# Optimization experiments

Hardware: AMD Instinct MI355X
Metric: run time of the kernel (lower is better)

## Reference

```python
import jax, jax.numpy as jnp
import numpy as np

B, L, VOCAB = 2, 1024, 32000
D = 512            # latent_dim
NL = 2             # num_layers
INNER = 2 * D      # mamba_expand * latent_dim
MLP = 2048         # mlp_inner_dim
NSEG = 8           # fixed number of subsequences (segment starts every SEG tokens)
SEG = L // NSEG


def setup_inputs() -> dict:
    key = jax.random.key(0)
    ks = jax.random.split(key, 12)
    decoder_output = jax.random.normal(ks[0], (B, L, VOCAB), jnp.float32) * 0.02
    input_ids = jax.random.randint(ks[1], (B, L, 1), 0, VOCAB)
    segmentation_indices = jnp.zeros((B, L, 1), jnp.int32).at[:, jnp.arange(0, L, SEG), :].set(1)
    E = jax.random.normal(ks[2], (VOCAB, D), jnp.float32) * 0.02          # tied embedding
    A = jax.random.uniform(ks[3], (NL, INNER), jnp.float32, 0.9, 0.999)   # per-channel SSM decay
    Win = jax.random.normal(ks[4], (NL, D, 2 * INNER), jnp.float32) * (D ** -0.5)
    Wout = jax.random.normal(ks[5], (NL, INNER, D), jnp.float32) * (INNER ** -0.5)
    Wm1 = jax.random.normal(ks[6], (NL, D, MLP), jnp.float32) * (D ** -0.5)
    Wm2 = jax.random.normal(ks[7], (NL, MLP, D), jnp.float32) * (MLP ** -0.5)
    mu_W = jax.random.normal(ks[8], (D, D), jnp.float32) * (D ** -0.5)
    mu_b = jnp.zeros((D,), jnp.float32)
    lv_W = jax.random.normal(ks[9], (D, D), jnp.float32) * (D ** -0.5)
    lv_b = jnp.zeros((D,), jnp.float32)
    return dict(decoder_output=decoder_output, input_ids=input_ids,
                segmentation_indices=segmentation_indices, E=E, A=A, Win=Win,
                Wout=Wout, Wm1=Wm1, Wm2=Wm2, mu_W=mu_W, mu_b=mu_b, lv_W=lv_W, lv_b=lv_b)


def _recurrence(a, u):
    # linear SSM recurrence h_t = a * h_{t-1} + u_t ; u: (..., L, INNER)
    u_t = jnp.moveaxis(u, -2, 0)
    h0 = jnp.zeros(u_t.shape[1:], u.dtype)
    def step(h, ut):
        h = a * h + ut
        return h, h
    _, hs = jax.lax.scan(step, h0, u_t)
    return jnp.moveaxis(hs, 0, -2)


def _seq_mixer(x, A, Win, Wout, Wm1, Wm2):
    # causal Mamba-style encoder: gated linear recurrence block + MLP block, residual
    for l in range(NL):
        u, g = jnp.split(x @ Win[l], 2, axis=-1)
        h = _recurrence(A[l], u)
        x = x + (jax.nn.silu(g) * h) @ Wout[l]
        x = x + jax.nn.silu(x @ Wm1[l]) @ Wm2[l]
    return x


def reference(decoder_output, input_ids, segmentation_indices, E, A, Win, Wout, Wm1, Wm2, mu_W, mu_b, lv_W, lv_b):
    correct = E[input_ids[..., 0]]                          # (B,L,D) ground-truth embeddings
    dec = jnp.einsum('blv,vd->bld', decoder_output, E)      # tied-linear projection of logits
    mask = segmentation_indices[..., 0].astype(bool)        # (B,L)
    starts = jax.vmap(lambda m: jnp.nonzero(m, size=NSEG)[0])(mask)        # (B,NSEG)
    ends = jnp.concatenate([starts[:, 1:], jnp.full((B, 1), L, starts.dtype)], axis=1)
    pos = jnp.arange(L)
    use_c = pos[None, None, :] < starts[:, :, None]                        # context region
    use_d = (pos[None, None, :] >= starts[:, :, None]) & (pos[None, None, :] < ends[:, :, None])
    # subsequence i = correct-embedding context [0,start_i) ++ decoder segment [start_i,end_i), zero-padded to L
    x = jnp.where(use_c[..., None], correct[:, None], 0.0) + jnp.where(use_d[..., None], dec[:, None], 0.0)  # (B,NSEG,L,D)
    h = _seq_mixer(x, A, Win, Wout, Wm1, Wm2)
    idx = (ends - 1)[:, :, None, None]                                     # last valid position per subsequence
    last = jnp.take_along_axis(h, idx, axis=2)[:, :, 0, :]                 # (B,NSEG,D)
    mu_q = last @ mu_W + mu_b
    logvar_q = last @ lv_W + lv_b
    return mu_q, logvar_q
```

## Files before the change

### kernel.cpp

```cpp
#include <hip/hip_runtime.h>
#include <hip/hip_bf16.h>
#include <math.h>


typedef short bf16x8 __attribute__((ext_vector_type(8)));
typedef float f32x4 __attribute__((ext_vector_type(4)));
typedef unsigned short u16;
typedef unsigned int u32;

#define AMODE_F32  0
#define AMODE_SILU 1
#define AMODE_BF16 2
#define EPI_STORE  0
#define EPI_ADD    1
#define EPI_SILU16 2

__device__ __forceinline__ u16 f2bf(float x) {
  u32 u = __float_as_uint(x);
  u += 0x7fffu + ((u >> 16) & 1u);
  return (u16)(u >> 16);
}
__device__ __forceinline__ float silu_f(float x) { return x / (1.f + expf(-x)); }

__device__ __forceinline__ void gload_lds16(const u16* g, u16* l) {
  __builtin_amdgcn_global_load_lds(
      (const u32 __attribute__((address_space(1)))*)(uintptr_t)(const void*)g,
      (u32 __attribute__((address_space(3)))*)(u32)(uintptr_t)(void*)l,
      16, 0, 0);
}

template<int RI, int RJ>
__global__ __launch_bounds__(256) void gemm_t(
    const void* __restrict__ Aptr, long lda, int amode,
    const float* __restrict__ Gptr, long ldg,
    const u16* __restrict__ Bt, long ldb,
    float* __restrict__ C, long ldc, long strideCz,
    u16* __restrict__ O16, long ldo,
    int Ks, int epi)
{
  constexpr int AR = RI * 32, BR = RJ * 32;
  __shared__ u16 As[AR * 64];
  __shared__ u16 Bs[BR * 64];
  const int t = threadIdx.x;
  const int row0 = blockIdx.y * AR;
  const int col0 = blockIdx.x * BR;
  const int kbeg = blockIdx.z * Ks;
  const int w = t >> 6, lane = t & 63;
  const int wr = (w >> 1) * (RI * 16), wc = (w & 1) * (RJ * 16);
  const int lm = lane & 15, qd = lane >> 4;
  const int swz = lm & 7;
  const int rg = lane >> 3;
  const int gsrc = (lane & 7) ^ (rg & 7);

  if (C) C += (long)blockIdx.z * strideCz;

  f32x4 acc[RI][RJ];
#pragma unroll
  for (int i = 0; i < RI; i++)
#pragma unroll
    for (int j = 0; j < RJ; j++) acc[i][j] = (f32x4)0.f;

  for (int kt = 0; kt < Ks; kt += 64) {
    const int k0 = kbeg + kt;
    {
      const u16* sp = Bt + (long)(col0 + rg) * ldb + k0 + gsrc * 8;
#pragma unroll
      for (int it = 0; it < RJ; it++) {
        int grp = w + it * 4;
        gload_lds16(sp + (long)(grp * 8) * ldb, Bs + grp * 512);
      }
    }
    if (amode == AMODE_BF16) {
      const u16* Ab = (const u16*)Aptr;
      const u16* sp = Ab + (long)(row0 + rg) * lda + k0 + gsrc * 8;
#pragma unroll
      for (int it = 0; it < RI; it++) {
        int grp = w + it * 4;
        gload_lds16(sp + (long)(grp * 8) * lda, As + grp * 512);
      }
    } else if (amode == AMODE_F32) {
      const float* A = (const float*)Aptr;
#pragma unroll
      for (int s = 0; s < RI * 2; s++) {
        int q = t + s * 256;
        int r = q >> 4, idx = q & 15;
        int g = idx >> 1, hh = idx & 1;
        const float4 v = *(const float4*)(A + (long)(row0 + r) * lda + k0 + g * 8 + hh * 4);
        ushort4 o; o.x = f2bf(v.x); o.y = f2bf(v.y); o.z = f2bf(v.z); o.w = f2bf(v.w);
        *(ushort4*)(As + r * 64 + ((g ^ (r & 7)) << 3) + hh * 4) = o;
      }
    } else {
      const float* H = (const float*)Aptr;
#pragma unroll
      for (int s = 0; s < RI * 2; s++) {
        int q = t + s * 256;
        int r = q >> 4, idx = q & 15;
        int g = idx >> 1, hh = idx & 1;
        long ro = (long)(row0 + r);
        const float4 gv = *(const float4*)(Gptr + ro * ldg + k0 + g * 8 + hh * 4);
        const float4 hv = *(const float4*)(H + ro * lda + k0 + g * 8 + hh * 4);
        ushort4 o;
        o.x = f2bf(silu_f(gv.x) * hv.x);
        o.y = f2bf(silu_f(gv.y) * hv.y);
        o.z = f2bf(silu_f(gv.z) * hv.z);
        o.w = f2bf(silu_f(gv.w) * hv.w);
        *(ushort4*)(As + r * 64 + ((g ^ (r & 7)) << 3) + hh * 4) = o;
      }
    }
    __syncthreads();
#pragma unroll
    for (int ks = 0; ks < 2; ks++) {
      bf16x8 af[RI], bg[RJ];
      const int p = ((ks * 4 + qd) ^ swz) << 3;
#pragma unroll
      for (int i = 0; i < RI; i++)
        af[i] = *(const bf16x8*)(As + (wr + 16 * i + lm) * 64 + p);
#pragma unroll
      for (int j = 0; j < RJ; j++)
        bg[j] = *(const bf16x8*)(Bs + (wc + 16 * j + lm) * 64 + p);
#pragma unroll
      for (int i = 0; i < RI; i++)
#pragma unroll
        for (int j = 0; j < RJ; j++)
          acc[i][j] = __builtin_amdgcn_mfma_f32_16x16x32_bf16(af[i], bg[j], acc[i][j], 0, 0, 0);
    }
    __syncthreads();
  }
#pragma unroll
  for (int i = 0; i < RI; i++)
#pragma unroll
    for (int j = 0; j < RJ; j++)
#pragma unroll
      for (int e = 0; e < 4; e++) {
        int row = row0 + wr + 16 * i + qd * 4 + e;
        int col = col0 + wc + 16 * j + lm;
        float v = acc[i][j][e];
        if (epi == EPI_STORE)      C[(long)row * ldc + col] = v;
        else if (epi == EPI_ADD)   C[(long)row * ldc + col] += v;
        else                       O16[(long)row * ldo + col] = f2bf(silu_f(v));
      }
}

__device__ __forceinline__ void tcast_body(const float* src, u16* dst, int R, int C) {
  __shared__ float tile[32][33];
  int c0 = blockIdx.x * 32, r0 = blockIdx.y * 32;
  if (c0 >= C || r0 >= R) return;
  int tc = threadIdx.x & 31, tr = threadIdx.x >> 5;
#pragma unroll
  for (int i = 0; i < 4; i++) {
    int r = tr + i * 8;
    tile[r][tc] = src[(long)(r0 + r) * C + c0 + tc];
  }
  __syncthreads();
#pragma unroll
  for (int i = 0; i < 4; i++) {
    int cc = tr + i * 8;
    dst[(long)(c0 + cc) * R + r0 + tc] = f2bf(tile[tc][cc]);
  }
}
__global__ __launch_bounds__(256) void tcast_k(const float* __restrict__ src, u16* __restrict__ dst, int R, int C) {
  tcast_body(src, dst, R, C);
}
__global__ __launch_bounds__(256) void tcast_w_k(
    const float* __restrict__ Win, const float* __restrict__ Wout,
    const float* __restrict__ Wm1, const float* __restrict__ Wm2,
    u16* __restrict__ WinT, u16* __restrict__ WoutT,
    u16* __restrict__ Wm1T, u16* __restrict__ Wm2T)
{
  int z = blockIdx.z; int l = z & 1; int which = z >> 1;
  const float* src; u16* dst; int R, C;
  if (which == 0)      { R = 512;  C = 2048; src = Win  + (long)l * R * C; dst = WinT  + (long)l * R * C; }
  else if (which == 1) { R = 1024; C = 512;  src = Wout + (long)l * R * C; dst = WoutT + (long)l * R * C; }
  else if (which == 2) { R = 512;  C = 2048; src = Wm1  + (long)l * R * C; dst = Wm1T  + (long)l * R * C; }
  else                 { R = 2048; C = 512;  src = Wm2  + (long)l * R * C; dst = Wm2T  + (long)l * R * C; }
  tcast_body(src, dst, R, C);
}

__global__ __launch_bounds__(128) void gather_k(const float* __restrict__ E, const int* __restrict__ ids,
                                                float* __restrict__ X) {
  int r = blockIdx.x;
  int id = ids[r];
  const float4* s = (const float4*)(E + (long)id * 512);
  float4* d = (float4*)(X + (long)r * 512);
  d[threadIdx.x] = s[threadIdx.x];
}

__global__ __launch_bounds__(256) void reduce_k(const float* __restrict__ P, float* __restrict__ X) {
  long i = (long)blockIdx.x * 256 + threadIdx.x;
  float s = 0.f;
#pragma unroll
  for (int z = 0; z < 10; z++) s += P[(long)z * 2048 * 512 + i];
  X[(long)2048 * 512 + i] = s;
}

__global__ __launch_bounds__(1024) void scanA_local_k(const float* __restrict__ ug, float* __restrict__ h,
                                                      const float* __restrict__ Ad, int l) {
  int b = blockIdx.x >> 3, ch = blockIdx.x & 7;
  int c = threadIdx.x;
  float a = Ad[l * 1024 + c];
  float hv = 0.f;
  long base = (long)b * 1024 + ch * 128;
  for (int t = 0; t < 128; t++) {
    long r = base + t;
    hv = a * hv + ug[r * 2048 + c];
    h[r * 1024 + c] = hv;
  }
}
__global__ __launch_bounds__(1024) void scanA_carry_k(const float* __restrict__ h, const float* __restrict__ Ad,
                                                      float* __restrict__ chk, int l) {
  int b = blockIdx.x, c = threadIdx.x;
  float a = Ad[l * 1024 + c];
  float p = a;
#pragma unroll
  for (int i = 0; i < 7; i++) p = p * p;
  float carry = 0.f;
  for (int i = 0; i < 8; i++) {
    chk[(((long)(b * 8 + i) * 2 + l) * 1024) + c] = carry;
    carry = p * carry + h[((long)b * 1024 + i * 128 + 127) * 1024 + c];
  }
}
__global__ __launch_bounds__(1024) void scan_fixB_k(const float* __restrict__ ug, float* __restrict__ h,
                                                    const float* __restrict__ Ad, const float* __restrict__ chk, int l) {
  int id = blockIdx.x, c = threadIdx.x;
  float a = Ad[l * 1024 + c];
  if (id < 16) {
    int b = id >> 3, ch = id & 7;
    if (ch == 0) return;
    float carry = chk[(((long)(b * 8 + ch) * 2 + l) * 1024) + c];
    float p = a;
    long base = (long)b * 1024 + ch * 128;
    for (int t = 0; t < 128; t++) {
      h[(base + t) * 1024 + c] += p * carry;
      p *= a;
    }
  } else {
    int q = id - 16; int b = q >> 3, sg = q & 7;
    float hv = chk[(((long)(b * 8 + sg) * 2 + l) * 1024) + c];
    long base = 2048 + (long)b * 1024 + sg * 128;
    for (int t = 0; t < 128; t++) {
      long r = base + t;
      hv = a * hv + ug[r * 2048 + c];
      h[r * 1024 + c] = hv;
    }
  }
}

__global__ __launch_bounds__(512) void head_k(const float* __restrict__ xB,
                                              const float* __restrict__ muW, const float* __restrict__ mub,
                                              const float* __restrict__ lvW, const float* __restrict__ lvb,
                                              float* __restrict__ out) {
  __shared__ float xs[512];
  int bi = blockIdx.x; int b = bi >> 3, i = bi & 7;
  long r = (long)b * 1024 + i * 128 + 127;
  xs[threadIdx.x] = xB[r * 512 + threadIdx.x];
  __syncthreads();
  int n = threadIdx.x;
  float mu = mub[n], lv = lvb[n];
  for (int k = 0; k < 512; k++) {
    float x = xs[k];
    mu += x * muW[(long)k * 512 + n];
    lv += x * lvW[(long)k * 512 + n];
  }
  out[(long)bi * 512 + n] = mu;
  out[8192 + (long)bi * 512 + n] = lv;
}

extern "C" void kernel_launch(void* const* d_in, const int* in_sizes, int n_in,
                              void* d_out, int out_size, void* d_ws, size_t ws_size,
                              hipStream_t stream) {
  const float* decoder = (const float*)d_in[0];
  const int*   ids     = (const int*)d_in[1];
  const float* E    = (const float*)d_in[3];
  const float* Adec = (const float*)d_in[4];
  const float* Win  = (const float*)d_in[5];
  const float* Wout = (const float*)d_in[6];
  const float* Wm1  = (const float*)d_in[7];
  const float* Wm2  = (const float*)d_in[8];
  const float* muW  = (const float*)d_in[9];
  const float* mub  = (const float*)d_in[10];
  const float* lvW  = (const float*)d_in[11];
  const float* lvb  = (const float*)d_in[12];
  float* out = (float*)d_out;

  char* ws = (char*)d_ws;
  size_t off = 0;
  auto alloc = [&](size_t bytes) { void* p = ws + off; off += (bytes + 255) & ~(size_t)255; return p; };
  float* X     = (float*)alloc((size_t)4096 * 512 * 4);
  float* ug    = (float*)alloc((size_t)4096 * 2048 * 4);
  float* hbuf  = (float*)alloc((size_t)4096 * 1024 * 4);
  u16*   m1    = (u16*)  alloc((size_t)4096 * 2048 * 2);
  float* chk   = (float*)alloc((size_t)2 * 8 * 2 * 1024 * 4);
  u16*   EbT   = (u16*)  alloc((size_t)512 * 32000 * 2);
  u16*   WinT  = (u16*)  alloc((size_t)2 * 512 * 2048 * 2);
  u16*   WoutT = (u16*)  alloc((size_t)2 * 1024 * 512 * 2);
  u16*   Wm1T  = (u16*)  alloc((size_t)2 * 512 * 2048 * 2);
  u16*   Wm2T  = (u16*)  alloc((size_t)2 * 2048 * 512 * 2);
  float* P     = ug;
  (void)ws_size; (void)in_sizes; (void)n_in; (void)out_size;

  tcast_k<<<dim3(16, 1000), 256, 0, stream>>>(E, EbT, 32000, 512);
  tcast_w_k<<<dim3(64, 64, 8), 256, 0, stream>>>(Win, Wout, Wm1, Wm2, WinT, WoutT, Wm1T, Wm2T);
  gather_k<<<2048, 128, 0, stream>>>(E, ids, X);

  gemm_t<2, 4><<<dim3(4, 32, 10), 256, 0, stream>>>(
      decoder, 32000, AMODE_F32, nullptr, 0, EbT, 32000,
      P, 512, (long)2048 * 512, nullptr, 0, 3200, EPI_STORE);
  reduce_k<<<4096, 256, 0, stream>>>(P, X);

  for (int l = 0; l < 2; l++) {
    gemm_t<4, 4><<<dim3(16, 32, 1), 256, 0, stream>>>(
        X, 512, AMODE_F32, nullptr, 0, WinT + (long)l * 2048 * 512, 512,
        ug, 2048, 0, nullptr, 0, 512, EPI_STORE);
    scanA_local_k<<<16, 1024, 0, stream>>>(ug, hbuf, Adec, l);
    scanA_carry_k<<<2, 1024, 0, stream>>>(hbuf, Adec, chk, l);
    scan_fixB_k<<<32, 1024, 0, stream>>>(ug, hbuf, Adec, chk, l);
    gemm_t<2, 2><<<dim3(8, 64, 1), 256, 0, stream>>>(
        hbuf, 1024, AMODE_SILU, ug + 1024, 2048, WoutT + (long)l * 512 * 1024, 1024,
        X, 512, 0, nullptr, 0, 1024, EPI_ADD);
    gemm_t<4, 4><<<dim3(16, 32, 1), 256, 0, stream>>>(
        X, 512, AMODE_F32, nullptr, 0, Wm1T + (long)l * 2048 * 512, 512,
        nullptr, 0, 0, m1, 2048, 512, EPI_SILU16);
    gemm_t<2, 2><<<dim3(8, 64, 1), 256, 0, stream>>>(
        m1, 2048, AMODE_BF16, nullptr, 0, Wm2T + (long)l * 512 * 2048, 2048,
        X, 512, 0, nullptr, 0, 2048, EPI_ADD);
  }

  head_k<<<16, 512, 0, stream>>>(X + (long)2048 * 512, muW, mub, lvW, lvb, out);
}
```

Before: 1.018 ms.

## Replace LDS-tiled GEMM with register-direct skinny GEMM and restructure SSM scan

The shared-memory tiled GEMM is replaced by a simpler kernel. Each wave computes a 16-row by RJ*16-column tile, loading A and B fragments straight from global memory into MFMA operands with no LDS or barriers. This gives many more, smaller blocks for occupancy. The three-kernel scan is replaced by a chunk-end pass and a gated pass that recomputes the carry per chunk, fuses silu(g)*h, and writes bf16 directly. This removes the fp32 h buffer and the silu work in the Wout GEMM's A-load. The head kernel is split across 32 blocks. The risk is lost data reuse, since each wave reloads B from global/L2 without LDS sharing, and the large vocab GEMM may become bandwidth-bound.

```diff
diff --git a/kernel.cpp b/kernel.cpp
--- a/kernel.cpp
+++ b/kernel.cpp
@@ -9,8 +9,7 @@
 typedef unsigned int u32;
 
 #define AMODE_F32  0
-#define AMODE_SILU 1
-#define AMODE_BF16 2
+#define AMODE_BF16 1
 #define EPI_STORE  0
 #define EPI_ADD    1
 #define EPI_SILU16 2
@@ -22,123 +21,65 @@
 }
 __device__ __forceinline__ float silu_f(float x) { return x / (1.f + expf(-x)); }
 
-__device__ __forceinline__ void gload_lds16(const u16* g, u16* l) {
-  __builtin_amdgcn_global_load_lds(
-      (const u32 __attribute__((address_space(1)))*)(uintptr_t)(const void*)g,
-      (u32 __attribute__((address_space(3)))*)(u32)(uintptr_t)(void*)l,
-      16, 0, 0);
-}
-
-template<int RI, int RJ>
-__global__ __launch_bounds__(256) void gemm_t(
-    const void* __restrict__ Aptr, long lda, int amode,
-    const float* __restrict__ Gptr, long ldg,
+template<int RJ, int AM, int EP>
+__global__ __launch_bounds__(256, 4) void sgemm(
+    const void* __restrict__ Aptr, long lda,
     const u16* __restrict__ Bt, long ldb,
     float* __restrict__ C, long ldc, long strideCz,
-    u16* __restrict__ O16, long ldo,
-    int Ks, int epi)
+    u16* __restrict__ O16, long ldo, int Ks)
 {
-  constexpr int AR = RI * 32, BR = RJ * 32;
-  __shared__ u16 As[AR * 64];
-  __shared__ u16 Bs[BR * 64];
   const int t = threadIdx.x;
-  const int row0 = blockIdx.y * AR;
-  const int col0 = blockIdx.x * BR;
-  const int kbeg = blockIdx.z * Ks;
   const int w = t >> 6, lane = t & 63;
-  const int wr = (w >> 1) * (RI * 16), wc = (w & 1) * (RJ * 16);
   const int lm = lane & 15, qd = lane >> 4;
-  const int swz = lm & 7;
-  const int rg = lane >> 3;
-  const int gsrc = (lane & 7) ^ (rg & 7);
-
-  if (C) C += (long)blockIdx.z * strideCz;
-
-  f32x4 acc[RI][RJ];
-#pragma unroll
-  for (int i = 0; i < RI; i++)
-#pragma unroll
-    for (int j = 0; j < RJ; j++) acc[i][j] = (f32x4)0.f;
-
-  for (int kt = 0; kt < Ks; kt += 64) {
-    const int k0 = kbeg + kt;
-    {
-      const u16* sp = Bt + (long)(col0 + rg) * ldb + k0 + gsrc * 8;
-#pragma unroll
-      for (int it = 0; it < RJ; it++) {
-        int grp = w + it * 4;
-        gload_lds16(sp + (long)(grp * 8) * ldb, Bs + grp * 512);
-      }
+  const int row0 = blockIdx.y * 16;
+  const int col0 = blockIdx.x * (RJ * 64) + w * (RJ * 16);
+  const long kbeg = (long)blockIdx.z * Ks;
+  if (EP == EPI_STORE) C += (long)blockIdx.z * strideCz;
+
+  f32x4 acc[RJ];
+#pragma unroll
+  for (int j = 0; j < RJ; j++) acc[j] = (f32x4)0.f;
+
+  const u16* bp[RJ];
+#pragma unroll
+  for (int j = 0; j < RJ; j++)
+    bp[j] = Bt + (long)(col0 + j * 16 + lm) * ldb + kbeg + qd * 8;
+
+  const float* apf = (const float*)Aptr + (long)(row0 + lm) * lda + kbeg + qd * 8;
+  const u16*  ap16 = (const u16*)Aptr + (long)(row0 + lm) * lda + kbeg + qd * 8;
+
+#pragma unroll 2
+  for (int kk = 0; kk < Ks; kk += 32) {
+    bf16x8 af;
+    if (AM == AMODE_F32) {
+      const float4 x = *(const float4*)(apf + kk);
+      const float4 y = *(const float4*)(apf + kk + 4);
+      af[0] = (short)f2bf(x.x); af[1] = (short)f2bf(x.y);
+      af[2] = (short)f2bf(x.z); af[3] = (short)f2bf(x.w);
+      af[4] = (short)f2bf(y.x); af[5] = (short)f2bf(y.y);
+      af[6] = (short)f2bf(y.z); af[7] = (short)f2bf(y.w);
+    } else {
+      af = *(const bf16x8*)(ap16 + kk);
     }
-    if (amode == AMODE_BF16) {
-      const u16* Ab = (const u16*)Aptr;
-      const u16* sp = Ab + (long)(row0 + rg) * lda + k0 + gsrc * 8;
-#pragma unroll
-      for (int it = 0; it < RI; it++) {
-        int grp = w + it * 4;
-        gload_lds16(sp + (long)(grp * 8) * lda, As + grp * 512);
-      }
-    } else if (amode == AMODE_F32) {
-      const float* A = (const float*)Aptr;
-#pragma unroll
-      for (int s = 0; s < RI * 2; s++) {
-        int q = t + s * 256;
-        int r = q >> 4, idx = q & 15;
-        int g = idx >> 1, hh = idx & 1;
-        const float4 v = *(const float4*)(A + (long)(row0 + r) * lda + k0 + g * 8 + hh * 4);
-        ushort4 o; o.x = f2bf(v.x); o.y = f2bf(v.y); o.z = f2bf(v.z); o.w = f2bf(v.w);
-        *(ushort4*)(As + r * 64 + ((g ^ (r & 7)) << 3) + hh * 4) = o;
-      }
-    } else {
-      const float* H = (const float*)Aptr;
-#pragma unroll
-      for (int s = 0; s < RI * 2; s++) {
-        int q = t + s * 256;
-        int r = q >> 4, idx = q & 15;
-        int g = idx >> 1, hh = idx & 1;
-        long ro = (long)(row0 + r);
-        const float4 gv = *(const float4*)(Gptr + ro * ldg + k0 + g * 8 + hh * 4);
-        const float4 hv = *(const float4*)(H + ro * lda + k0 + g * 8 + hh * 4);
-        ushort4 o;
-        o.x = f2bf(silu_f(gv.x) * hv.x);
-        o.y = f2bf(silu_f(gv.y) * hv.y);
-        o.z = f2bf(silu_f(gv.z) * hv.z);
-        o.w = f2bf(silu_f(gv.w) * hv.w);
-        *(ushort4*)(As + r * 64 + ((g ^ (r & 7)) << 3) + hh * 4) = o;
-      }
+#pragma unroll
+    for (int j = 0; j < RJ; j++) {
+      const bf16x8 bf = *(const bf16x8*)(bp[j] + kk);
+      acc[j] = __builtin_amdgcn_mfma_f32_16x16x32_bf16(af, bf, acc[j], 0, 0, 0);
     }
-    __syncthreads();
-#pragma unroll
-    for (int ks = 0; ks < 2; ks++) {
-      bf16x8 af[RI], bg[RJ];
-      const int p = ((ks * 4 + qd) ^ swz) << 3;
-#pragma unroll
-      for (int i = 0; i < RI; i++)
-        af[i] = *(const bf16x8*)(As + (wr + 16 * i + lm) * 64 + p);
-#pragma unroll
-      for (int j = 0; j < RJ; j++)
-        bg[j] = *(const bf16x8*)(Bs + (wc + 16 * j + lm) * 64 + p);
-#pragma unroll
-      for (int i = 0; i < RI; i++)
-#pragma unroll
-        for (int j = 0; j < RJ; j++)
-          acc[i][j] = __builtin_amdgcn_mfma_f32_16x16x32_bf16(af[i], bg[j], acc[i][j], 0, 0, 0);
+  }
+
+#pragma unroll
+  for (int j = 0; j < RJ; j++) {
+    const int col = col0 + j * 16 + lm;
+#pragma unroll
+    for (int e = 0; e < 4; e++) {
+      const int row = row0 + qd * 4 + e;
+      const float v = acc[j][e];
+      if (EP == EPI_STORE)     C[(long)row * ldc + col] = v;
+      else if (EP == EPI_ADD)  C[(long)row * ldc + col] += v;
+      else                     O16[(long)row * ldo + col] = f2bf(silu_f(v));
     }
-    __syncthreads();
-  }
-#pragma unroll
-  for (int i = 0; i < RI; i++)
-#pragma unroll
-    for (int j = 0; j < RJ; j++)
-#pragma unroll
-      for (int e = 0; e < 4; e++) {
-        int row = row0 + wr + 16 * i + qd * 4 + e;
-        int col = col0 + wc + 16 * j + lm;
-        float v = acc[i][j][e];
-        if (epi == EPI_STORE)      C[(long)row * ldc + col] = v;
-        else if (epi == EPI_ADD)   C[(long)row * ldc + col] += v;
-        else                       O16[(long)row * ldo + col] = f2bf(silu_f(v));
-      }
+  }
 }
 
 __device__ __forceinline__ void tcast_body(const float* src, u16* dst, int R, int C) {
@@ -193,55 +134,34 @@
   X[(long)2048 * 512 + i] = s;
 }
 
-__global__ __launch_bounds__(1024) void scanA_local_k(const float* __restrict__ ug, float* __restrict__ h,
-                                                      const float* __restrict__ Ad, int l) {
-  int b = blockIdx.x >> 3, ch = blockIdx.x & 7;
-  int c = threadIdx.x;
+__global__ __launch_bounds__(256) void scan_ends_k(const float* __restrict__ ug, const float* __restrict__ Ad,
+                                                   float* __restrict__ ends, int l) {
+  int b = blockIdx.x >> 5, ch = (blockIdx.x >> 2) & 7;
+  int c = (blockIdx.x & 3) * 256 + threadIdx.x;
   float a = Ad[l * 1024 + c];
   float hv = 0.f;
   long base = (long)b * 1024 + ch * 128;
+  for (int t = 0; t < 128; t++) hv = a * hv + ug[(base + t) * 2048 + c];
+  ends[(b * 8 + ch) * 1024 + c] = hv;
+}
+__global__ __launch_bounds__(256) void scan_gate_k(const float* __restrict__ ug, const float* __restrict__ Ad,
+                                                   const float* __restrict__ ends, u16* __restrict__ hb, int l) {
+  int u = blockIdx.x >> 2;
+  int c = (blockIdx.x & 3) * 256 + threadIdx.x;
+  int pass = u >> 4, b = (u >> 3) & 1, ch = u & 7;
+  float a = Ad[l * 1024 + c];
+  float p128 = a;
+#pragma unroll
+  for (int i = 0; i < 7; i++) p128 = p128 * p128;
+  float hv = 0.f;
+  for (int i = 0; i < ch; i++) hv = p128 * hv + ends[(b * 8 + i) * 1024 + c];
+  long base = (long)pass * 2048 + (long)b * 1024 + ch * 128;
   for (int t = 0; t < 128; t++) {
     long r = base + t;
-    hv = a * hv + ug[r * 2048 + c];
-    h[r * 1024 + c] = hv;
-  }
-}
-__global__ __launch_bounds__(1024) void scanA_carry_k(const float* __restrict__ h, const float* __restrict__ Ad,
-                                                      float* __restrict__ chk, int l) {
-  int b = blockIdx.x, c = threadIdx.x;
-  float a = Ad[l * 1024 + c];
-  float p = a;
-#pragma unroll
-  for (int i = 0; i < 7; i++) p = p * p;
-  float carry = 0.f;
-  for (int i = 0; i < 8; i++) {
-    chk[(((long)(b * 8 + i) * 2 + l) * 1024) + c] = carry;
-    carry = p * carry + h[((long)b * 1024 + i * 128 + 127) * 1024 + c];
-  }
-}
-__global__ __launch_bounds__(1024) void scan_fixB_k(const float* __restrict__ ug, float* __restrict__ h,
-                                                    const float* __restrict__ Ad, const float* __restrict__ chk, int l) {
-  int id = blockIdx.x, c = threadIdx.x;
-  float a = Ad[l * 1024 + c];
-  if (id < 16) {
-    int b = id >> 3, ch = id & 7;
-    if (ch == 0) return;
-    float carry = chk[(((long)(b * 8 + ch) * 2 + l) * 1024) + c];
-    float p = a;
-    long base = (long)b * 1024 + ch * 128;
-    for (int t = 0; t < 128; t++) {
-      h[(base + t) * 1024 + c] += p * carry;
-      p *= a;
-    }
-  } else {
-    int q = id - 16; int b = q >> 3, sg = q & 7;
-    float hv = chk[(((long)(b * 8 + sg) * 2 + l) * 1024) + c];
-    long base = 2048 + (long)b * 1024 + sg * 128;
-    for (int t = 0; t < 128; t++) {
-      long r = base + t;
-      hv = a * hv + ug[r * 2048 + c];
-      h[r * 1024 + c] = hv;
-    }
+    float uu = ug[r * 2048 + c];
+    float g  = ug[r * 2048 + 1024 + c];
+    hv = a * hv + uu;
+    hb[r * 1024 + c] = f2bf(silu_f(g) * hv);
   }
 }
 
@@ -250,19 +170,17 @@
                                               const float* __restrict__ lvW, const float* __restrict__ lvb,
                                               float* __restrict__ out) {
   __shared__ float xs[512];
-  int bi = blockIdx.x; int b = bi >> 3, i = bi & 7;
+  int h = blockIdx.x >> 4, bi = blockIdx.x & 15;
+  int b = bi >> 3, i = bi & 7;
+  const float* W = h ? lvW : muW;
+  const float* bias = h ? lvb : mub;
   long r = (long)b * 1024 + i * 128 + 127;
   xs[threadIdx.x] = xB[r * 512 + threadIdx.x];
   __syncthreads();
   int n = threadIdx.x;
-  float mu = mub[n], lv = lvb[n];
-  for (int k = 0; k < 512; k++) {
-    float x = xs[k];
-    mu += x * muW[(long)k * 512 + n];
-    lv += x * lvW[(long)k * 512 + n];
-  }
-  out[(long)bi * 512 + n] = mu;
-  out[8192 + (long)bi * 512 + n] = lv;
+  float s = bias[n];
+  for (int k = 0; k < 512; k++) s += xs[k] * W[(long)k * 512 + n];
+  out[(long)h * 8192 + (long)bi * 512 + n] = s;
 }
 
 extern "C" void kernel_launch(void* const* d_in, const int* in_sizes, int n_in,
@@ -287,9 +205,9 @@
   auto alloc = [&](size_t bytes) { void* p = ws + off; off += (bytes + 255) & ~(size_t)255; return p; };
   float* X     = (float*)alloc((size_t)4096 * 512 * 4);
   float* ug    = (float*)alloc((size_t)4096 * 2048 * 4);
-  float* hbuf  = (float*)alloc((size_t)4096 * 1024 * 4);
+  u16*   hb16  = (u16*)  alloc((size_t)4096 * 1024 * 2);
   u16*   m1    = (u16*)  alloc((size_t)4096 * 2048 * 2);
-  float* chk   = (float*)alloc((size_t)2 * 8 * 2 * 1024 * 4);
+  float* ends  = (float*)alloc((size_t)2 * 8 * 1024 * 4);
   u16*   EbT   = (u16*)  alloc((size_t)512 * 32000 * 2);
   u16*   WinT  = (u16*)  alloc((size_t)2 * 512 * 2048 * 2);
   u16*   WoutT = (u16*)  alloc((size_t)2 * 1024 * 512 * 2);
@@ -302,28 +220,22 @@
   tcast_w_k<<<dim3(64, 64, 8), 256, 0, stream>>>(Win, Wout, Wm1, Wm2, WinT, WoutT, Wm1T, Wm2T);
   gather_k<<<2048, 128, 0, stream>>>(E, ids, X);
 
-  gemm_t<2, 4><<<dim3(4, 32, 10), 256, 0, stream>>>(
-      decoder, 32000, AMODE_F32, nullptr, 0, EbT, 32000,
-      P, 512, (long)2048 * 512, nullptr, 0, 3200, EPI_STORE);
+  sgemm<8, AMODE_F32, EPI_STORE><<<dim3(1, 128, 10), 256, 0, stream>>>(
+      decoder, 32000, EbT, 32000, P, 512, (long)2048 * 512, nullptr, 0, 3200);
   reduce_k<<<4096, 256, 0, stream>>>(P, X);
 
   for (int l = 0; l < 2; l++) {
-    gemm_t<4, 4><<<dim3(16, 32, 1), 256, 0, stream>>>(
-        X, 512, AMODE_F32, nullptr, 0, WinT + (long)l * 2048 * 512, 512,
-        ug, 2048, 0, nullptr, 0, 512, EPI_STORE);
-    scanA_local_k<<<16, 1024, 0, stream>>>(ug, hbuf, Adec, l);
-    scanA_carry_k<<<2, 1024, 0, stream>>>(hbuf, Adec, chk, l);
-    scan_fixB_k<<<32, 1024, 0, stream>>>(ug, hbuf, Adec, chk, l);
-    gemm_t<2, 2><<<dim3(8, 64, 1), 256, 0, stream>>>(
-        hbuf, 1024, AMODE_SILU, ug + 1024, 2048, WoutT + (long)l * 512 * 1024, 1024,
-        X, 512, 0, nullptr, 0, 1024, EPI_ADD);
-    gemm_t<4, 4><<<dim3(16, 32, 1), 256, 0, stream>>>(
-        X, 512, AMODE_F32, nullptr, 0, Wm1T + (long)l * 2048 * 512, 512,
-        nullptr, 0, 0, m1, 2048, 512, EPI_SILU16);
-    gemm_t<2, 2><<<dim3(8, 64, 1), 256, 0, stream>>>(
-        m1, 2048, AMODE_BF16, nullptr, 0, Wm2T + (long)l * 512 * 2048, 2048,
-        X, 512, 0, nullptr, 0, 2048, EPI_ADD);
-  }
-
-  head_k<<<16, 512, 0, stream>>>(X + (long)2048 * 512, muW, mub, lvW, lvb, out);
-}
+    sgemm<8, AMODE_F32, EPI_STORE><<<dim3(4, 256, 1), 256, 0, stream>>>(
+        X, 512, WinT + (long)l * 2048 * 512, 512, ug, 2048, 0, nullptr, 0, 512);
+    scan_ends_k<<<64, 256, 0, stream>>>(ug, Adec, ends, l);
+    scan_gate_k<<<128, 256, 0, stream>>>(ug, Adec, ends, hb16, l);
+    sgemm<2, AMODE_BF16, EPI_ADD><<<dim3(4, 256, 1), 256, 0, stream>>>(
+        hb16, 1024, WoutT + (long)l * 512 * 1024, 1024, X, 512, 0, nullptr, 0, 1024);
+    sgemm<8, AMODE_F32, EPI_SILU16><<<dim3(4, 256, 1), 256, 0, stream>>>(
+        X, 512, Wm1T + (long)l * 2048 * 512, 512, nullptr, 0, 0, m1, 2048, 512);
+    sgemm<2, AMODE_BF16, EPI_ADD><<<dim3(4, 256, 1), 256, 0, stream>>>(
+        m1, 2048, Wm2T + (long)l * 512 * 2048, 2048, X, 512, 0, nullptr, 0, 2048);
+  }
+
+  head_k<<<32, 512, 0, stream>>>(X + (long)2048 * 512, muW, mub, lvW, lvb, out);
+}
```

After: 1.657 ms. +62.7%, slower.

## Rewrite decoder GEMM with atomics, fuse scan with gating, retile mixer GEMMs

Applied to the files above, without the earlier changes.

The decoder-projection GEMM becomes a dedicated 1024-thread kernel with a 128x512 tile. It splits K into 20 chunks and accumulates with atomicAdd into a zeroed buffer, which removes the partial-sum buffer and reduce kernel. The three-kernel segmented scan is replaced by two kernels: one computes per-chunk end states, the other recomputes the carry-in, runs the recurrence and writes silu(g)*h directly as bf16. That removes the fp32 h buffer and the SILU A-mode from the GEMM. Mixer GEMMs switch to 2x8 warp tiles with occupancy hints, and the head kernel splits mu and logvar across blocks; atomics make results order-nondeterministic.

```diff
diff --git a/kernel.cpp b/kernel.cpp
--- a/kernel.cpp
+++ b/kernel.cpp
@@ -9,8 +9,7 @@
 typedef unsigned int u32;
 
 #define AMODE_F32  0
-#define AMODE_SILU 1
-#define AMODE_BF16 2
+#define AMODE_BF16 1
 #define EPI_STORE  0
 #define EPI_ADD    1
 #define EPI_SILU16 2
@@ -29,12 +28,82 @@
       16, 0, 0);
 }
 
+__global__ __launch_bounds__(1024, 4) void gemm_dec(
+    const float* __restrict__ A,
+    const u16* __restrict__ Bt,
+    float* __restrict__ C)
+{
+  __shared__ u16 As[128 * 64];
+  __shared__ u16 Bs[512 * 64];
+  const int t = threadIdx.x;
+  const int w = t >> 6, lane = t & 63;
+  const int lm = lane & 15, qd = lane >> 4;
+  const int swz = lm & 7;
+  const int rg = lane >> 3;
+  const int gsrc = (lane & 7) ^ (rg & 7);
+  const int row0 = blockIdx.y * 128;
+  const long kbeg = (long)blockIdx.z * 1600;
+  const int wr = (w >> 3) * 64, wc = (w & 7) * 64;
+
+  f32x4 acc[4][4];
+#pragma unroll
+  for (int i = 0; i < 4; i++)
+#pragma unroll
+    for (int j = 0; j < 4; j++) acc[i][j] = (f32x4)0.f;
+
+  const u16* bsp = Bt + (long)rg * 32000 + kbeg + gsrc * 8;
+
+  for (int kt = 0; kt < 1600; kt += 64) {
+#pragma unroll
+    for (int it = 0; it < 4; it++) {
+      int grp = w + it * 16;
+      gload_lds16(bsp + (long)(grp * 8) * 32000 + kt, Bs + grp * 512);
+    }
+#pragma unroll
+    for (int s = 0; s < 2; s++) {
+      int q = t + s * 1024;
+      int r = q >> 4, idx = q & 15;
+      int g = idx >> 1, hh = idx & 1;
+      const float4 v = *(const float4*)(A + (long)(row0 + r) * 32000 + kbeg + kt + g * 8 + hh * 4);
+      ushort4 o; o.x = f2bf(v.x); o.y = f2bf(v.y); o.z = f2bf(v.z); o.w = f2bf(v.w);
+      *(ushort4*)(As + r * 64 + ((g ^ (r & 7)) << 3) + hh * 4) = o;
+    }
+    __syncthreads();
+#pragma unroll
+    for (int ks = 0; ks < 2; ks++) {
+      bf16x8 af[4], bg[4];
+      const int p = ((ks * 4 + qd) ^ swz) << 3;
+#pragma unroll
+      for (int i = 0; i < 4; i++)
+        af[i] = *(const bf16x8*)(As + (wr + 16 * i + lm) * 64 + p);
+#pragma unroll
+      for (int j = 0; j < 4; j++)
+        bg[j] = *(const bf16x8*)(Bs + (wc + 16 * j + lm) * 64 + p);
+#pragma unroll
+      for (int i = 0; i < 4; i++)
+#pragma unroll
+        for (int j = 0; j < 4; j++)
+          acc[i][j] = __builtin_amdgcn_mfma_f32_16x16x32_bf16(af[i], bg[j], acc[i][j], 0, 0, 0);
+    }
+    __syncthreads();
+  }
+#pragma unroll
+  for (int i = 0; i < 4; i++)
+#pragma unroll
+    for (int j = 0; j < 4; j++)
+#pragma unroll
+      for (int e = 0; e < 4; e++) {
+        int row = row0 + wr + 16 * i + qd * 4 + e;
+        int col = wc + 16 * j + lm;
+        atomicAdd(C + (long)row * 512 + col, acc[i][j][e]);
+      }
+}
+
 template<int RI, int RJ>
-__global__ __launch_bounds__(256) void gemm_t(
+__global__ __launch_bounds__(256, 4) void gemm_t(
     const void* __restrict__ Aptr, long lda, int amode,
-    const float* __restrict__ Gptr, long ldg,
     const u16* __restrict__ Bt, long ldb,
-    float* __restrict__ C, long ldc, long strideCz,
+    float* __restrict__ C, long ldc,
     u16* __restrict__ O16, long ldo,
     int Ks, int epi)
 {
@@ -44,7 +113,6 @@
   const int t = threadIdx.x;
   const int row0 = blockIdx.y * AR;
   const int col0 = blockIdx.x * BR;
-  const int kbeg = blockIdx.z * Ks;
   const int w = t >> 6, lane = t & 63;
   const int wr = (w >> 1) * (RI * 16), wc = (w & 1) * (RJ * 16);
   const int lm = lane & 15, qd = lane >> 4;
@@ -52,8 +120,6 @@
   const int rg = lane >> 3;
   const int gsrc = (lane & 7) ^ (rg & 7);
 
-  if (C) C += (long)blockIdx.z * strideCz;
-
   f32x4 acc[RI][RJ];
 #pragma unroll
   for (int i = 0; i < RI; i++)
@@ -61,7 +127,7 @@
     for (int j = 0; j < RJ; j++) acc[i][j] = (f32x4)0.f;
 
   for (int kt = 0; kt < Ks; kt += 64) {
-    const int k0 = kbeg + kt;
+    const int k0 = kt;
     {
       const u16* sp = Bt + (long)(col0 + rg) * ldb + k0 + gsrc * 8;
 #pragma unroll
@@ -78,7 +144,7 @@
         int grp = w + it * 4;
         gload_lds16(sp + (long)(grp * 8) * lda, As + grp * 512);
       }
-    } else if (amode == AMODE_F32) {
+    } else {
       const float* A = (const float*)Aptr;
 #pragma unroll
       for (int s = 0; s < RI * 2; s++) {
@@ -87,23 +153,6 @@
         int g = idx >> 1, hh = idx & 1;
         const float4 v = *(const float4*)(A + (long)(row0 + r) * lda + k0 + g * 8 + hh * 4);
         ushort4 o; o.x = f2bf(v.x); o.y = f2bf(v.y); o.z = f2bf(v.z); o.w = f2bf(v.w);
-        *(ushort4*)(As + r * 64 + ((g ^ (r & 7)) << 3) + hh * 4) = o;
-      }
-    } else {
-      const float* H = (const float*)Aptr;
-#pragma unroll
-      for (int s = 0; s < RI * 2; s++) {
-        int q = t + s * 256;
-        int r = q >> 4, idx = q & 15;
-        int g = idx >> 1, hh = idx & 1;
-        long ro = (long)(row0 + r);
-        const float4 gv = *(const float4*)(Gptr + ro * ldg + k0 + g * 8 + hh * 4);
-        const float4 hv = *(const float4*)(H + ro * lda + k0 + g * 8 + hh * 4);
-        ushort4 o;
-        o.x = f2bf(silu_f(gv.x) * hv.x);
-        o.y = f2bf(silu_f(gv.y) * hv.y);
-        o.z = f2bf(silu_f(gv.z) * hv.z);
-        o.w = f2bf(silu_f(gv.w) * hv.w);
         *(ushort4*)(As + r * 64 + ((g ^ (r & 7)) << 3) + hh * 4) = o;
       }
     }
@@ -185,62 +234,46 @@
   d[threadIdx.x] = s[threadIdx.x];
 }
 
-__global__ __launch_bounds__(256) void reduce_k(const float* __restrict__ P, float* __restrict__ X) {
-  long i = (long)blockIdx.x * 256 + threadIdx.x;
-  float s = 0.f;
-#pragma unroll
-  for (int z = 0; z < 10; z++) s += P[(long)z * 2048 * 512 + i];
-  X[(long)2048 * 512 + i] = s;
-}
-
-__global__ __launch_bounds__(1024) void scanA_local_k(const float* __restrict__ ug, float* __restrict__ h,
-                                                      const float* __restrict__ Ad, int l) {
-  int b = blockIdx.x >> 3, ch = blockIdx.x & 7;
-  int c = threadIdx.x;
+__global__ __launch_bounds__(256) void scan_ends_k(const float* __restrict__ ug, const float* __restrict__ Ad,
+                                                   float* __restrict__ ends, int l) {
+  int b = blockIdx.x >> 5, ch = (blockIdx.x >> 2) & 7;
+  int c = (blockIdx.x & 3) * 256 + threadIdx.x;
   float a = Ad[l * 1024 + c];
   float hv = 0.f;
   long base = (long)b * 1024 + ch * 128;
-  for (int t = 0; t < 128; t++) {
-    long r = base + t;
-    hv = a * hv + ug[r * 2048 + c];
-    h[r * 1024 + c] = hv;
-  }
-}
-__global__ __launch_bounds__(1024) void scanA_carry_k(const float* __restrict__ h, const float* __restrict__ Ad,
-                                                      float* __restrict__ chk, int l) {
-  int b = blockIdx.x, c = threadIdx.x;
+  for (int t0 = 0; t0 < 128; t0 += 8) {
+    float uu[8];
+#pragma unroll
+    for (int j = 0; j < 8; j++) uu[j] = ug[(base + t0 + j) * 2048 + c];
+#pragma unroll
+    for (int j = 0; j < 8; j++) hv = a * hv + uu[j];
+  }
+  ends[(b * 8 + ch) * 1024 + c] = hv;
+}
+__global__ __launch_bounds__(256) void scan_gate_k(const float* __restrict__ ug, const float* __restrict__ Ad,
+                                                   const float* __restrict__ ends, u16* __restrict__ hb, int l) {
+  int u = blockIdx.x >> 2;
+  int c = (blockIdx.x & 3) * 256 + threadIdx.x;
+  int pass = u >> 4, b = (u >> 3) & 1, ch = u & 7;
   float a = Ad[l * 1024 + c];
-  float p = a;
-#pragma unroll
-  for (int i = 0; i < 7; i++) p = p * p;
-  float carry = 0.f;
-  for (int i = 0; i < 8; i++) {
-    chk[(((long)(b * 8 + i) * 2 + l) * 1024) + c] = carry;
-    carry = p * carry + h[((long)b * 1024 + i * 128 + 127) * 1024 + c];
-  }
-}
-__global__ __launch_bounds__(1024) void scan_fixB_k(const float* __restrict__ ug, float* __restrict__ h,
-                                                    const float* __restrict__ Ad, const float* __restrict__ chk, int l) {
-  int id = blockIdx.x, c = threadIdx.x;
-  float a = Ad[l * 1024 + c];
-  if (id < 16) {
-    int b = id >> 3, ch = id & 7;
-    if (ch == 0) return;
-    float carry = chk[(((long)(b * 8 + ch) * 2 + l) * 1024) + c];
-    float p = a;
-    long base = (long)b * 1024 + ch * 128;
-    for (int t = 0; t < 128; t++) {
-      h[(base + t) * 1024 + c] += p * carry;
-      p *= a;
-    }
-  } else {
-    int q = id - 16; int b = q >> 3, sg = q & 7;
-    float hv = chk[(((long)(b * 8 + sg) * 2 + l) * 1024) + c];
-    long base = 2048 + (long)b * 1024 + sg * 128;
-    for (int t = 0; t < 128; t++) {
-      long r = base + t;
-      hv = a * hv + ug[r * 2048 + c];
-      h[r * 1024 + c] = hv;
+  float p128 = a;
+#pragma unroll
+  for (int i = 0; i < 7; i++) p128 = p128 * p128;
+  float hv = 0.f;
+  for (int i = 0; i < ch; i++) hv = p128 * hv + ends[(b * 8 + i) * 1024 + c];
+  long base = (long)pass * 2048 + (long)b * 1024 + ch * 128;
+  for (int t0 = 0; t0 < 128; t0 += 8) {
+    float uu[8], gg[8];
+#pragma unroll
+    for (int j = 0; j < 8; j++) {
+      long r = base + t0 + j;
+      uu[j] = ug[r * 2048 + c];
+      gg[j] = ug[r * 2048 + 1024 + c];
+    }
+#pragma unroll
+    for (int j = 0; j < 8; j++) {
+      hv = a * hv + uu[j];
+      hb[(base + t0 + j) * 1024 + c] = f2bf(silu_f(gg[j]) * hv);
     }
   }
 }
@@ -250,19 +283,18 @@
                                               const float* __restrict__ lvW, const float* __restrict__ lvb,
                                               float* __restrict__ out) {
   __shared__ float xs[512];
-  int bi = blockIdx.x; int b = bi >> 3, i = bi & 7;
+  int h = blockIdx.x >> 4, bi = blockIdx.x & 15;
+  int b = bi >> 3, i = bi & 7;
+  const float* W = h ? lvW : muW;
+  const float* bias = h ? lvb : mub;
   long r = (long)b * 1024 + i * 128 + 127;
   xs[threadIdx.x] = xB[r * 512 + threadIdx.x];
   __syncthreads();
   int n = threadIdx.x;
-  float mu = mub[n], lv = lvb[n];
-  for (int k = 0; k < 512; k++) {
-    float x = xs[k];
-    mu += x * muW[(long)k * 512 + n];
-    lv += x * lvW[(long)k * 512 + n];
-  }
-  out[(long)bi * 512 + n] = mu;
-  out[8192 + (long)bi * 512 + n] = lv;
+  float s = bias[n];
+#pragma unroll 8
+  for (int k = 0; k < 512; k++) s += xs[k] * W[(long)k * 512 + n];
+  out[(long)h * 8192 + (long)bi * 512 + n] = s;
 }
 
 extern "C" void kernel_launch(void* const* d_in, const int* in_sizes, int n_in,
@@ -287,43 +319,39 @@
   auto alloc = [&](size_t bytes) { void* p = ws + off; off += (bytes + 255) & ~(size_t)255; return p; };
   float* X     = (float*)alloc((size_t)4096 * 512 * 4);
   float* ug    = (float*)alloc((size_t)4096 * 2048 * 4);
-  float* hbuf  = (float*)alloc((size_t)4096 * 1024 * 4);
+  u16*   hb16  = (u16*)  alloc((size_t)4096 * 1024 * 2);
   u16*   m1    = (u16*)  alloc((size_t)4096 * 2048 * 2);
-  float* chk   = (float*)alloc((size_t)2 * 8 * 2 * 1024 * 4);
+  float* ends  = (float*)alloc((size_t)2 * 8 * 1024 * 4);
   u16*   EbT   = (u16*)  alloc((size_t)512 * 32000 * 2);
   u16*   WinT  = (u16*)  alloc((size_t)2 * 512 * 2048 * 2);
   u16*   WoutT = (u16*)  alloc((size_t)2 * 1024 * 512 * 2);
   u16*   Wm1T  = (u16*)  alloc((size_t)2 * 512 * 2048 * 2);
   u16*   Wm2T  = (u16*)  alloc((size_t)2 * 2048 * 512 * 2);
-  float* P     = ug;
   (void)ws_size; (void)in_sizes; (void)n_in; (void)out_size;
 
   tcast_k<<<dim3(16, 1000), 256, 0, stream>>>(E, EbT, 32000, 512);
   tcast_w_k<<<dim3(64, 64, 8), 256, 0, stream>>>(Win, Wout, Wm1, Wm2, WinT, WoutT, Wm1T, Wm2T);
+  hipMemsetAsync(X + (size_t)2048 * 512, 0, (size_t)2048 * 512 * 4, stream);
   gather_k<<<2048, 128, 0, stream>>>(E, ids, X);
 
-  gemm_t<2, 4><<<dim3(4, 32, 10), 256, 0, stream>>>(
-      decoder, 32000, AMODE_F32, nullptr, 0, EbT, 32000,
-      P, 512, (long)2048 * 512, nullptr, 0, 3200, EPI_STORE);
-  reduce_k<<<4096, 256, 0, stream>>>(P, X);
+  gemm_dec<<<dim3(1, 16, 20), 1024, 0, stream>>>(decoder, EbT, X + (size_t)2048 * 512);
 
   for (int l = 0; l < 2; l++) {
-    gemm_t<4, 4><<<dim3(16, 32, 1), 256, 0, stream>>>(
-        X, 512, AMODE_F32, nullptr, 0, WinT + (long)l * 2048 * 512, 512,
-        ug, 2048, 0, nullptr, 0, 512, EPI_STORE);
-    scanA_local_k<<<16, 1024, 0, stream>>>(ug, hbuf, Adec, l);
-    scanA_carry_k<<<2, 1024, 0, stream>>>(hbuf, Adec, chk, l);
-    scan_fixB_k<<<32, 1024, 0, stream>>>(ug, hbuf, Adec, chk, l);
-    gemm_t<2, 2><<<dim3(8, 64, 1), 256, 0, stream>>>(
-        hbuf, 1024, AMODE_SILU, ug + 1024, 2048, WoutT + (long)l * 512 * 1024, 1024,
-        X, 512, 0, nullptr, 0, 1024, EPI_ADD);
-    gemm_t<4, 4><<<dim3(16, 32, 1), 256, 0, stream>>>(
-        X, 512, AMODE_F32, nullptr, 0, Wm1T + (long)l * 2048 * 512, 512,
-        nullptr, 0, 0, m1, 2048, 512, EPI_SILU16);
-    gemm_t<2, 2><<<dim3(8, 64, 1), 256, 0, stream>>>(
-        m1, 2048, AMODE_BF16, nullptr, 0, Wm2T + (long)l * 512 * 2048, 2048,
-        X, 512, 0, nullptr, 0, 2048, EPI_ADD);
-  }
-
-  head_k<<<16, 512, 0, stream>>>(X + (long)2048 * 512, muW, mub, lvW, lvb, out);
-}
+    gemm_t<2, 8><<<dim3(8, 64), 256, 0, stream>>>(
+        X, 512, AMODE_F32, WinT + (long)l * 2048 * 512, 512,
+        ug, 2048, nullptr, 0, 512, EPI_STORE);
+    scan_ends_k<<<64, 256, 0, stream>>>(ug, Adec, ends, l);
+    scan_gate_k<<<128, 256, 0, stream>>>(ug, Adec, ends, hb16, l);
+    gemm_t<2, 8><<<dim3(2, 64), 256, 0, stream>>>(
+        hb16, 1024, AMODE_BF16, WoutT + (long)l * 512 * 1024, 1024,
+        X, 512, nullptr, 0, 1024, EPI_ADD);
+    gemm_t<2, 8><<<dim3(8, 64), 256, 0, stream>>>(
+        X, 512, AMODE_F32, Wm1T + (long)l * 2048 * 512, 512,
+        nullptr, 0, m1, 2048, 512, EPI_SILU16);
+    gemm_t<2, 8><<<dim3(2, 64), 256, 0, stream>>>(
+        m1, 2048, AMODE_BF16, Wm2T + (long)l * 512 * 2048, 2048,
+        X, 512, nullptr, 0, 2048, EPI_ADD);
+  }
+
+  head_k<<<32, 512, 0, stream>>>(X + (long)2048 * 512, muW, mub, lvW, lvb, out);
+}
```

Result: no change. 1.003 ms (-1.5%).
